# Kernel optimization log

Hardware: AMD Instinct MI355X
Metric: run time of the kernel (lower is better)

The kernel has to match this reference:

```python
import jax, jax.numpy as jnp
import numpy as np

B, S, D, H, OUT = 512, 200, 64, 512, 1
EPS = 1e-5  # torch LayerNorm default


def ln(x, g, b, axes=-1):
    m = x.mean(axis=axes, keepdims=True)
    v = ((x - m) ** 2).mean(axis=axes, keepdims=True)
    return (x - m) * jax.lax.rsqrt(v + EPS) * g + b


def lstm_layer(xs, W_ih, b_ih, W_hh, b_hh, g_ih, be_ih, g_hh, be_hh, g_ho, be_ho):
    # xs: (S, B, in_dim) -> (S, B, H)
    nb = xs.shape[1]
    def step(carry, x_t):
        h, c = carry
        gates = ln(x_t @ W_ih.T + b_ih, g_ih, be_ih) + ln(h @ W_hh.T + b_hh, g_hh, be_hh)
        i, f, g, o = jnp.split(gates, 4, axis=-1)
        c_new = jax.nn.sigmoid(f) * c + jax.nn.sigmoid(i) * jnp.tanh(g)
        h_new = jax.nn.sigmoid(o) * ln(jnp.tanh(c_new), g_ho, be_ho)
        return (h_new, c_new), h_new
    init = (jnp.zeros((nb, H), xs.dtype), jnp.zeros((nb, H), xs.dtype))
    _, hs = jax.lax.scan(step, init, xs)
    return hs


def setup_inputs() -> dict:
    key = jax.random.key(0)
    ks = iter(jax.random.split(key, 16))
    scale = 0.02
    def rn(shape):
        return jax.random.normal(next(ks), shape, jnp.float32) * scale
    inp = {"x": jax.random.normal(next(ks), (B, S, D), jnp.float32)}
    inp["ln1_g"] = jnp.ones((S, D), jnp.float32)
    inp["ln1_b"] = jnp.zeros((S, D), jnp.float32)
    for l, ind in ((0, D), (1, H)):
        inp[f"W_ih{l}"] = rn((4 * H, ind)); inp[f"b_ih{l}"] = jnp.zeros((4 * H,), jnp.float32)
        inp[f"W_hh{l}"] = rn((4 * H, H));  inp[f"b_hh{l}"] = jnp.zeros((4 * H,), jnp.float32)
        inp[f"g_ih{l}"] = jnp.ones((4 * H,), jnp.float32); inp[f"be_ih{l}"] = jnp.zeros((4 * H,), jnp.float32)
        inp[f"g_hh{l}"] = jnp.ones((4 * H,), jnp.float32); inp[f"be_hh{l}"] = jnp.zeros((4 * H,), jnp.float32)
        inp[f"g_ho{l}"] = jnp.ones((H,), jnp.float32);     inp[f"be_ho{l}"] = jnp.zeros((H,), jnp.float32)
    inp["Wd1"] = rn((H // 4, H));      inp["bd1"] = jnp.zeros((H // 4,), jnp.float32)
    inp["Wd2"] = rn((H // 8, H // 4)); inp["bd2"] = jnp.zeros((H // 8,), jnp.float32)
    inp["Wd3"] = rn((H // 16, H // 8)); inp["bd3"] = jnp.zeros((H // 16,), jnp.float32)
    inp["Wd4"] = rn((OUT, H // 16));   inp["bd4"] = jnp.zeros((OUT,), jnp.float32)
    return inp


def _forward(x, ln1_g, ln1_b,
             W_ih0, b_ih0, W_hh0, b_hh0, g_ih0, be_ih0, g_hh0, be_hh0, g_ho0, be_ho0,
             W_ih1, b_ih1, W_hh1, b_hh1, g_ih1, be_ih1, g_hh1, be_hh1, g_ho1, be_ho1,
             Wd1, bd1, Wd2, bd2, Wd3, bd3, Wd4, bd4):
    # ln1 normalizes jointly over (seq_len, input_dim)
    x = ln(x, ln1_g, ln1_b, axes=(-2, -1))
    xs = jnp.transpose(x, (1, 0, 2))  # (S, B, D)
    hs = lstm_layer(xs, W_ih0, b_ih0, W_hh0, b_hh0, g_ih0, be_ih0, g_hh0, be_hh0, g_ho0, be_ho0)
    hs = lstm_layer(hs, W_ih1, b_ih1, W_hh1, b_hh1, g_ih1, be_ih1, g_hh1, be_hh1, g_ho1, be_ho1)
    h_last = hs[-1]  # (B, H): last_num=1, eval-mode dropout is identity
    z = jax.nn.relu(h_last @ Wd1.T + bd1)
    z = jax.nn.relu(z @ Wd2.T + bd2)
    z = jax.nn.relu(z @ Wd3.T + bd3)
    return z @ Wd4.T + bd4  # (B, OUT)


def reference(x, ln1_g, ln1_b,
              W_ih0, b_ih0, W_hh0, b_hh0, g_ih0, be_ih0, g_hh0, be_hh0, g_ho0, be_ho0,
              W_ih1, b_ih1, W_hh1, b_hh1, g_ih1, be_ih1, g_hh1, be_hh1, g_ho1, be_ho1,
              Wd1, bd1, Wd2, bd2, Wd3, bd3, Wd4, bd4):
    return _forward(x, ln1_g, ln1_b,
                    W_ih0, b_ih0, W_hh0, b_hh0, g_ih0, be_ih0, g_hh0, be_hh0, g_ho0, be_ho0,
                    W_ih1, b_ih1, W_hh1, b_hh1, g_ih1, be_ih1, g_hh1, be_hh1, g_ho1, be_ho1,
                    Wd1, bd1, Wd2, bd2, Wd3, bd3, Wd4, bd4)
```

## Files before the change

### kernel.cpp

```cpp
#include <hip/hip_runtime.h>
#include <math.h>

#define BATCH 512
#define SEQ   200
#define DIN   64
#define HID   512
#define GW    2048
#define EPS   1e-5f
#define NREG  4

typedef _Float16 half_t;
typedef half_t half8 __attribute__((ext_vector_type(8)));
typedef float  f32x4  __attribute__((ext_vector_type(4)));
typedef float  f32x16 __attribute__((ext_vector_type(16)));

#define WN0 (2048*64)
#define WN1 (2048*512)
#define WTOT (WN0 + 3*WN1)

__device__ __forceinline__ float sigf(float x){ return 1.0f/(1.0f+expf(-x)); }

__device__ __forceinline__ void block_reduce4(float&a,float&b,float&c,float&d,float* red){
  #pragma unroll
  for(int o=32;o;o>>=1){
    a+=__shfl_down(a,o); b+=__shfl_down(b,o);
    c+=__shfl_down(c,o); d+=__shfl_down(d,o);
  }
  const int lane = threadIdx.x & 63, wid = threadIdx.x>>6;
  if(lane==0){ red[wid*4+0]=a; red[wid*4+1]=b; red[wid*4+2]=c; red[wid*4+3]=d; }
  __syncthreads();
  a = red[0]+red[4]+red[8]+red[12];
  b = red[1]+red[5]+red[9]+red[13];
  c = red[2]+red[6]+red[10]+red[14];
  d = red[3]+red[7]+red[11]+red[15];
  __syncthreads();
}

__global__ __launch_bounds__(256) void ln1_stats(const float* __restrict__ x,
                                                 float* __restrict__ mu,
                                                 float* __restrict__ rs){
  const int b = blockIdx.x;
  const float* xb = x + (size_t)b*SEQ*DIN;
  float s=0, ss=0, d=0, e=0;
  for (int i=threadIdx.x; i<SEQ*DIN; i+=256){ float v=xb[i]; s+=v; ss+=v*v; }
  __shared__ float red[16];
  block_reduce4(s,ss,d,e,red);
  if (threadIdx.x==0){
    float m = s*(1.0f/(SEQ*DIN));
    mu[b] = m;
    rs[b] = rsqrtf(ss*(1.0f/(SEQ*DIN)) - m*m + EPS);
  }
}

__global__ __launch_bounds__(256) void wsplit(
    const float* __restrict__ W0, const float* __restrict__ W1,
    const float* __restrict__ W2, const float* __restrict__ W3,
    half_t* __restrict__ Wh, half_t* __restrict__ Wl)
{
  int i = blockIdx.x*256 + threadIdx.x;
  if (i >= WTOT) return;
  const float* src; int off, Kd;
  if (i < WN0){ src=W0; off=i; Kd=DIN; }
  else {
    int r = (i-WN0)/WN1; off = (i-WN0) - r*WN1; Kd=HID;
    src = (r==0)?W1:((r==1)?W2:W3);
  }
  const int C = Kd>>5;
  int j  = off & 7;
  int l  = (off>>3) & 63;
  int ks = (off>>9) & 1;
  int nf = (off>>10) & 1;
  int pc = off>>11;
  int c  = pc & (C-1);
  int p  = pc >> (Kd==DIN ? 1 : 4);
  int n  = p*64 + nf*32 + (l&31);
  int k  = c*32 + ks*16 + (l>>5)*8 + j;
  float v = src[(size_t)n*Kd + k];
  half_t h = (half_t)v;
  Wh[i] = h;
  Wl[i] = (half_t)(v - (float)h);
}

__global__ __launch_bounds__(256) void tick_mm32(
    const float* __restrict__ x, const float* __restrict__ g1, const float* __restrict__ b1,
    const float* __restrict__ mu, const float* __restrict__ rsg,
    const half_t* __restrict__ h0fh, const half_t* __restrict__ h0fl,
    const half_t* __restrict__ h1fh, const half_t* __restrict__ h1fl,
    const half_t* __restrict__ Wh, const half_t* __restrict__ Wl,
    float* __restrict__ G, int t)
{
  const int z    = blockIdx.z;
  const int tid  = threadIdx.x;
  const int lane = tid & 63;
  const int w    = tid >> 6;
  const int ln31 = lane & 31;
  const int lk8  = (lane >> 5) << 3;

  const int wm0 = blockIdx.y*64 + (w>>1)*32;
  const int wn0 = blockIdx.x*128 + (w&1)*64;
  const int p   = blockIdx.x*2 + (w&1);
  const int mch = wm0 >> 5;

  const half_t* Bh = Wh + WN0; const half_t* Bl = Wl + WN0;
  const half_t* FAh = h0fh;    const half_t* FAl = h0fl;
  int Kd = HID;
  if (z==0){ Bh=Wh; Bl=Wl; Kd=DIN; }
  else if (z==2){ Bh=Wh+WN0+WN1; Bl=Wl+WN0+WN1; }
  else if (z==3){ FAh=h1fh; FAl=h1fl; Bh=Wh+WN0+2*WN1; Bl=Wl+WN0+2*WN1; }

  const int C32 = Kd >> 5;
  const int C16 = Kd >> 4;

  const half_t* Bph = Bh + (size_t)p*C32*2048 + lane*8;
  const half_t* Bpl = Bl + (size_t)p*C32*2048 + lane*8;
  const half_t* Aph = FAh + (size_t)mch*HID*32 + lane*8;
  const half_t* Apl = FAl + (size_t)mch*HID*32 + lane*8;

  const int tq = (t < SEQ) ? t : (SEQ-1);

  const int arow = wm0 + ln31;
  float m_=0.f, r_=0.f;
  const float *xr=nullptr, *gr=nullptr, *br=nullptr;
  if (z==0){
    m_ = mu[arow]; r_ = rsg[arow];
    xr = x  + (size_t)arow*(SEQ*DIN) + (size_t)tq*DIN + lk8;
    gr = g1 + (size_t)tq*DIN + lk8;
    br = b1 + (size_t)tq*DIN + lk8;
  }

  f32x16 acc0 = {0.f,0.f,0.f,0.f,0.f,0.f,0.f,0.f,0.f,0.f,0.f,0.f,0.f,0.f,0.f,0.f};
  f32x16 acc1 = acc0;

  struct Frag { half8 ah, al, bh0, bh1, bl0, bl1; };
  auto loadF = [&](int c16)->Frag{
    Frag f;
    if (z==0){
      const float* xp = xr + c16*16;
      const float* gp = gr + c16*16;
      const float* bp = br + c16*16;
      #pragma unroll
      for (int j=0;j<8;j++){
        float v = (xp[j]-m_)*r_*gp[j] + bp[j];
        half_t hv = (half_t)v;
        f.ah[j] = hv; f.al[j] = (half_t)(v - (float)hv);
      }
    } else {
      f.ah = *(const half8*)(Aph + (size_t)c16*512);
      f.al = *(const half8*)(Apl + (size_t)c16*512);
    }
    const size_t boff = (size_t)(c16>>1)*2048 + (size_t)(c16&1)*512;
    f.bh0 = *(const half8*)(Bph + boff);
    f.bh1 = *(const half8*)(Bph + boff + 1024);
    f.bl0 = *(const half8*)(Bpl + boff);
    f.bl1 = *(const half8*)(Bpl + boff + 1024);
    return f;
  };
  auto mmstep = [&](const Frag& f){
    acc0 = __builtin_amdgcn_mfma_f32_32x32x16_f16(f.ah, f.bh0, acc0, 0,0,0);
    acc1 = __builtin_amdgcn_mfma_f32_32x32x16_f16(f.ah, f.bh1, acc1, 0,0,0);
    acc0 = __builtin_amdgcn_mfma_f32_32x32x16_f16(f.al, f.bh0, acc0, 0,0,0);
    acc1 = __builtin_amdgcn_mfma_f32_32x32x16_f16(f.al, f.bh1, acc1, 0,0,0);
    acc0 = __builtin_amdgcn_mfma_f32_32x32x16_f16(f.ah, f.bl0, acc0, 0,0,0);
    acc1 = __builtin_amdgcn_mfma_f32_32x32x16_f16(f.ah, f.bl1, acc1, 0,0,0);
  };

  Frag Fa = loadF(0);
  for (int c=0; c<C16; c+=2){
    Frag Fb = loadF(c+1);
    mmstep(Fa);
    if (c+2 < C16) Fa = loadF(c+2);
    mmstep(Fb);
  }

  float* Gr = G + (size_t)z*BATCH*GW + (size_t)0;
  const int rbase = (lane>>5)<<2;
  #pragma unroll
  for (int reg=0; reg<16; reg++){
    const int m = wm0 + (reg&3) + ((reg>>2)<<3) + rbase;
    __builtin_nontemporal_store(acc0[reg], &Gr[(size_t)m*GW + wn0 + ln31]);
    __builtin_nontemporal_store(acc1[reg], &Gr[(size_t)m*GW + wn0 + 32 + ln31]);
  }
}

__global__ __launch_bounds__(256) void tick_update(
    const float* __restrict__ G,
    const float* __restrict__ b_ih0, const float* __restrict__ b_hh0,
    const float* __restrict__ b_ih1, const float* __restrict__ b_hh1,
    const float* __restrict__ g_ih0, const float* __restrict__ be_ih0,
    const float* __restrict__ g_hh0, const float* __restrict__ be_hh0,
    const float* __restrict__ g_ho0, const float* __restrict__ be_ho0,
    const float* __restrict__ g_ih1, const float* __restrict__ be_ih1,
    const float* __restrict__ g_hh1, const float* __restrict__ be_hh1,
    const float* __restrict__ g_ho1, const float* __restrict__ be_ho1,
    float* __restrict__ h0, float* __restrict__ c0,
    float* __restrict__ h1, float* __restrict__ c1,
    half_t* __restrict__ h0fh, half_t* __restrict__ h0fl,
    half_t* __restrict__ h1fh, half_t* __restrict__ h1fl, int t)
{
  const int layer = blockIdx.x >> 9;
  const int b = blockIdx.x & 511;
  if (layer==0 && t>=SEQ) return;
  if (layer==1 && t==0)   return;

  const float *GA,*GB,*bA,*bB,*gA,*beA,*gB,*beB,*gH,*bH;
  float *cs,*hs; half_t *hfx,*lfx;
  const size_t rb = (size_t)b*GW;
  if (layer==0){
    GA = G + rb;
    GB = G + (size_t)1*BATCH*GW + rb;
    bA=b_ih0; bB=b_hh0;
    gA=g_ih0; beA=be_ih0; gB=g_hh0; beB=be_hh0; gH=g_ho0; bH=be_ho0;
    cs = c0 + b*HID; hs = h0 + b*HID; hfx = h0fh; lfx = h0fl;
  } else {
    GA = G + (size_t)2*BATCH*GW + rb;
    GB = G + (size_t)3*BATCH*GW + rb;
    bA=b_ih1; bB=b_hh1;
    gA=g_ih1; beA=be_ih1; gB=g_hh1; beB=be_hh1; gH=g_ho1; bH=be_ho1;
    cs = c1 + b*HID; hs = h1 + b*HID; hfx = h1fh; lfx = h1fl;
  }

  const int tid = threadIdx.x;
  __shared__ float red[16];
  __shared__ __align__(16) float GS[2*GW];
  __shared__ float su[HID];
  __shared__ float so[HID];

  float sa=0, ssa=0, sb=0, ssb=0;
  for (int i=tid*4; i<GW; i+=1024){
    f32x4 va = *(const f32x4*)(GA+i);
    va += *(const f32x4*)(bA+i);
    *(f32x4*)(GS+i) = va;
    f32x4 vb = *(const f32x4*)(GB+i);
    vb += *(const f32x4*)(bB+i);
    *(f32x4*)(GS+GW+i) = vb;
    #pragma unroll
    for (int q=0;q<4;q++){
      sa += va[q]; ssa += va[q]*va[q];
      sb += vb[q]; ssb += vb[q]*vb[q];
    }
  }
  block_reduce4(sa,ssa,sb,ssb,red);
  const float ma = sa*(1.0f/GW);
  const float ra = rsqrtf(ssa*(1.0f/GW) - ma*ma + EPS);
  const float mb = sb*(1.0f/GW);
  const float rb_ = rsqrtf(ssb*(1.0f/GW) - mb*mb + EPS);

  float s_u=0, s_uu=0;
  for (int j=tid;j<HID;j+=256){
    float iv = ((GS[j      ]-ma)*ra*gA[j      ]+beA[j      ]) + ((GS[GW+j      ]-mb)*rb_*gB[j      ]+beB[j      ]);
    float fv = ((GS[j+  HID]-ma)*ra*gA[j+  HID]+beA[j+  HID]) + ((GS[GW+j+  HID]-mb)*rb_*gB[j+  HID]+beB[j+  HID]);
    float gv = ((GS[j+2*HID]-ma)*ra*gA[j+2*HID]+beA[j+2*HID]) + ((GS[GW+j+2*HID]-mb)*rb_*gB[j+2*HID]+beB[j+2*HID]);
    float ov = ((GS[j+3*HID]-ma)*ra*gA[j+3*HID]+beA[j+3*HID]) + ((GS[GW+j+3*HID]-mb)*rb_*gB[j+3*HID]+beB[j+3*HID]);
    float cn = sigf(fv)*cs[j] + sigf(iv)*tanhf(gv);
    cs[j] = cn;
    float u = tanhf(cn);
    su[j] = u; so[j] = sigf(ov);
    s_u += u; s_uu += u*u;
  }
  float d3=0,d4=0;
  block_reduce4(s_u,s_uu,d3,d4,red);
  const float mu_u = s_u*(1.0f/HID);
  const float ru   = rsqrtf(s_uu*(1.0f/HID) - mu_u*mu_u + EPS);

  const size_t fbase = ((size_t)(b>>5)*32)*512 + (size_t)(b&31)*8;
  for (int j=tid;j<HID;j+=256){
    float v = so[j] * ((su[j]-mu_u)*ru*gH[j] + bH[j]);
    hs[j] = v;
    half_t hv = (half_t)v;
    half_t lv = (half_t)(v - (float)hv);
    const size_t fi = fbase + (size_t)(j>>4)*512 + (size_t)((j>>3)&1)*256 + (j&7);
    hfx[fi] = hv;
    lfx[fi] = lv;
  }
}

__global__ __launch_bounds__(256) void head_kernel(
    const float* __restrict__ h1,
    const float* __restrict__ Wd1, const float* __restrict__ bd1,
    const float* __restrict__ Wd2, const float* __restrict__ bd2,
    const float* __restrict__ Wd3, const float* __restrict__ bd3,
    const float* __restrict__ Wd4, const float* __restrict__ bd4,
    float* __restrict__ out)
{
  const int b = blockIdx.x;
  __shared__ float hv[HID];
  __shared__ float z1[128];
  __shared__ float z2[64];
  __shared__ float z3[32];
  const int tid = threadIdx.x;
  for (int i=tid;i<HID;i+=256) hv[i]=h1[(size_t)b*HID+i];
  __syncthreads();
  if (tid<128){
    float acc=bd1[tid]; const float* w=Wd1+(size_t)tid*512;
    for(int k=0;k<512;k++) acc+=hv[k]*w[k];
    z1[tid]=fmaxf(acc,0.f);
  }
  __syncthreads();
  if (tid<64){
    float acc=bd2[tid]; const float* w=Wd2+(size_t)tid*128;
    for(int k=0;k<128;k++) acc+=z1[k]*w[k];
    z2[tid]=fmaxf(acc,0.f);
  }
  __syncthreads();
  if (tid<32){
    float acc=bd3[tid]; const float* w=Wd3+(size_t)tid*64;
    for(int k=0;k<64;k++) acc+=z2[k]*w[k];
    z3[tid]=fmaxf(acc,0.f);
  }
  __syncthreads();
  if (tid==0){
    float acc=bd4[0];
    for(int k=0;k<32;k++) acc+=z3[k]*Wd4[k];
    out[b]=acc;
  }
}

extern "C" void kernel_launch(void* const* d_in, const int* in_sizes, int n_in,
                              void* d_out, int out_size, void* d_ws, size_t ws_size,
                              hipStream_t stream) {
  const float* x      = (const float*)d_in[0];
  const float* ln1_g  = (const float*)d_in[1];
  const float* ln1_b  = (const float*)d_in[2];
  const float* W_ih0  = (const float*)d_in[3];
  const float* b_ih0  = (const float*)d_in[4];
  const float* W_hh0  = (const float*)d_in[5];
  const float* b_hh0  = (const float*)d_in[6];
  const float* g_ih0  = (const float*)d_in[7];
  const float* be_ih0 = (const float*)d_in[8];
  const float* g_hh0  = (const float*)d_in[9];
  const float* be_hh0 = (const float*)d_in[10];
  const float* g_ho0  = (const float*)d_in[11];
  const float* be_ho0 = (const float*)d_in[12];
  const float* W_ih1  = (const float*)d_in[13];
  const float* b_ih1  = (const float*)d_in[14];
  const float* W_hh1  = (const float*)d_in[15];
  const float* b_hh1  = (const float*)d_in[16];
  const float* g_ih1  = (const float*)d_in[17];
  const float* be_ih1 = (const float*)d_in[18];
  const float* g_hh1  = (const float*)d_in[19];
  const float* be_hh1 = (const float*)d_in[20];
  const float* g_ho1  = (const float*)d_in[21];
  const float* be_ho1 = (const float*)d_in[22];
  const float* Wd1    = (const float*)d_in[23];
  const float* bd1    = (const float*)d_in[24];
  const float* Wd2    = (const float*)d_in[25];
  const float* bd2    = (const float*)d_in[26];
  const float* Wd3    = (const float*)d_in[27];
  const float* bd3    = (const float*)d_in[28];
  const float* Wd4    = (const float*)d_in[29];
  const float* bd4    = (const float*)d_in[30];
  float* out = (float*)d_out;

  float* ws = (float*)d_ws;
  float* G  = ws;
  float* h0 = G  + NREG*(size_t)BATCH*GW;
  float* c0 = h0 + (size_t)BATCH*HID;
  float* h1 = c0 + (size_t)BATCH*HID;
  float* c1 = h1 + (size_t)BATCH*HID;
  half_t* h0fh = (half_t*)(c1 + (size_t)BATCH*HID);
  half_t* h0fl = h0fh + (size_t)BATCH*HID;
  half_t* h1fh = h0fl + (size_t)BATCH*HID;
  half_t* h1fl = h1fh + (size_t)BATCH*HID;
  float* mu = (float*)(h1fl + (size_t)BATCH*HID);
  float* rs = mu + BATCH;
  half_t* Wh = (half_t*)(rs + BATCH);
  half_t* Wl = Wh + (size_t)WTOT;

  hipMemsetAsync(h0, 0, 4*(size_t)BATCH*HID*4 + 4*(size_t)BATCH*HID*2, stream);

  ln1_stats<<<BATCH, 256, 0, stream>>>(x, mu, rs);
  wsplit<<<(WTOT+255)/256, 256, 0, stream>>>(W_ih0, W_hh0, W_ih1, W_hh1, Wh, Wl);

  dim3 mgrid(16, 8, NREG);
  for (int t = 0; t <= SEQ; ++t) {
    tick_mm32<<<mgrid, 256, 0, stream>>>(x, ln1_g, ln1_b, mu, rs,
        h0fh, h0fl, h1fh, h1fl, Wh, Wl, G, t);
    tick_update<<<dim3(1024), 256, 0, stream>>>(G,
        b_ih0, b_hh0, b_ih1, b_hh1,
        g_ih0, be_ih0, g_hh0, be_hh0, g_ho0, be_ho0,
        g_ih1, be_ih1, g_hh1, be_hh1, g_ho1, be_ho1,
        h0, c0, h1, c1, h0fh, h0fl, h1fh, h1fl, t);
  }
  head_kernel<<<BATCH, 256, 0, stream>>>(h1, Wd1, bd1, Wd2, bd2, Wd3, bd3, Wd4, bd4, out);
}
```

Measured before the change: 6.028 ms.

## Precompute normalized input fragments and enlarge per-wave MFMA tile to 64x64

Adds an xprep kernel that applies the joint layer norm to the input once for all timesteps, splits it into fp16 hi/lo parts, and stores them in MFMA fragment layout. The per-timestep GEMM kernel then only loads these fragments instead of recomputing the normalization every tick. Each wave now computes a 64x64 output tile (two row chunks times two column halves), so every loaded weight fragment is reused across twice as many rows, and the grid is halved. The cost is a larger workspace, more accumulator registers per wave (launch_bounds 256,1), and fewer blocks per launch (256 instead of 512), which lowers parallelism on a many-CU device.

```diff
diff --git a/kernel.cpp b/kernel.cpp
--- a/kernel.cpp
+++ b/kernel.cpp
@@ -17,6 +17,7 @@
 #define WN0 (2048*64)
 #define WN1 (2048*512)
 #define WTOT (WN0 + 3*WN1)
+#define XFRAG ((size_t)SEQ*16*4*512)
 
 __device__ __forceinline__ float sigf(float x){ return 1.0f/(1.0f+expf(-x)); }
 
@@ -81,9 +82,29 @@
   Wl[i] = (half_t)(v - (float)h);
 }
 
-__global__ __launch_bounds__(256) void tick_mm32(
+__global__ __launch_bounds__(256) void xprep(
     const float* __restrict__ x, const float* __restrict__ g1, const float* __restrict__ b1,
-    const float* __restrict__ mu, const float* __restrict__ rsg,
+    const float* __restrict__ mu, const float* __restrict__ rs,
+    half_t* __restrict__ xh, half_t* __restrict__ xl)
+{
+  size_t i = (size_t)blockIdx.x*256 + threadIdx.x;
+  if (i >= XFRAG) return;
+  int j   = (int)(i & 7);
+  int l   = (int)((i>>3) & 63);
+  int c   = (int)((i>>9) & 3);
+  int mch = (int)((i>>11) & 15);
+  int t   = (int)(i>>15);
+  int b   = mch*32 + (l&31);
+  int k   = c*16 + ((l>>5)<<3) + j;
+  float v = (x[(size_t)b*(SEQ*DIN) + t*DIN + k] - mu[b]) * rs[b]
+            * g1[t*DIN+k] + b1[t*DIN+k];
+  half_t h = (half_t)v;
+  xh[i] = h;
+  xl[i] = (half_t)(v - (float)h);
+}
+
+__global__ __launch_bounds__(256, 1) void tick_mm64(
+    const half_t* __restrict__ xh, const half_t* __restrict__ xl,
     const half_t* __restrict__ h0fh, const half_t* __restrict__ h0fl,
     const half_t* __restrict__ h1fh, const half_t* __restrict__ h1fl,
     const half_t* __restrict__ Wh, const half_t* __restrict__ Wl,
@@ -94,91 +115,91 @@
   const int lane = tid & 63;
   const int w    = tid >> 6;
   const int ln31 = lane & 31;
-  const int lk8  = (lane >> 5) << 3;
-
-  const int wm0 = blockIdx.y*64 + (w>>1)*32;
-  const int wn0 = blockIdx.x*128 + (w&1)*64;
-  const int p   = blockIdx.x*2 + (w&1);
-  const int mch = wm0 >> 5;
+
+  const int mch0 = blockIdx.y*2;
+  const int p    = blockIdx.x*4 + w;
+  const int wn0  = p*64;
 
   const half_t* Bh = Wh + WN0; const half_t* Bl = Wl + WN0;
-  const half_t* FAh = h0fh;    const half_t* FAl = h0fl;
   int Kd = HID;
   if (z==0){ Bh=Wh; Bl=Wl; Kd=DIN; }
   else if (z==2){ Bh=Wh+WN0+WN1; Bl=Wl+WN0+WN1; }
-  else if (z==3){ FAh=h1fh; FAl=h1fl; Bh=Wh+WN0+2*WN1; Bl=Wl+WN0+2*WN1; }
+  else if (z==3){ Bh=Wh+WN0+2*WN1; Bl=Wl+WN0+2*WN1; }
 
   const int C32 = Kd >> 5;
   const int C16 = Kd >> 4;
 
   const half_t* Bph = Bh + (size_t)p*C32*2048 + lane*8;
   const half_t* Bpl = Bl + (size_t)p*C32*2048 + lane*8;
-  const half_t* Aph = FAh + (size_t)mch*HID*32 + lane*8;
-  const half_t* Apl = FAl + (size_t)mch*HID*32 + lane*8;
 
   const int tq = (t < SEQ) ? t : (SEQ-1);
-
-  const int arow = wm0 + ln31;
-  float m_=0.f, r_=0.f;
-  const float *xr=nullptr, *gr=nullptr, *br=nullptr;
+  const half_t *Aph0,*Apl0,*Aph1,*Apl1;
   if (z==0){
-    m_ = mu[arow]; r_ = rsg[arow];
-    xr = x  + (size_t)arow*(SEQ*DIN) + (size_t)tq*DIN + lk8;
-    gr = g1 + (size_t)tq*DIN + lk8;
-    br = b1 + (size_t)tq*DIN + lk8;
-  }
-
-  f32x16 acc0 = {0.f,0.f,0.f,0.f,0.f,0.f,0.f,0.f,0.f,0.f,0.f,0.f,0.f,0.f,0.f,0.f};
-  f32x16 acc1 = acc0;
-
-  struct Frag { half8 ah, al, bh0, bh1, bl0, bl1; };
-  auto loadF = [&](int c16)->Frag{
-    Frag f;
-    if (z==0){
-      const float* xp = xr + c16*16;
-      const float* gp = gr + c16*16;
-      const float* bp = br + c16*16;
-      #pragma unroll
-      for (int j=0;j<8;j++){
-        float v = (xp[j]-m_)*r_*gp[j] + bp[j];
-        half_t hv = (half_t)v;
-        f.ah[j] = hv; f.al[j] = (half_t)(v - (float)hv);
-      }
-    } else {
-      f.ah = *(const half8*)(Aph + (size_t)c16*512);
-      f.al = *(const half8*)(Apl + (size_t)c16*512);
-    }
-    const size_t boff = (size_t)(c16>>1)*2048 + (size_t)(c16&1)*512;
-    f.bh0 = *(const half8*)(Bph + boff);
-    f.bh1 = *(const half8*)(Bph + boff + 1024);
-    f.bl0 = *(const half8*)(Bpl + boff);
-    f.bl1 = *(const half8*)(Bpl + boff + 1024);
+    const size_t xb = ((size_t)tq*16 + mch0)*2048 + lane*8;
+    Aph0 = xh + xb; Aph1 = xh + xb + 2048;
+    Apl0 = xl + xb; Apl1 = xl + xb + 2048;
+  } else {
+    const half_t* FAh = (z==3) ? h1fh : h0fh;
+    const half_t* FAl = (z==3) ? h1fl : h0fl;
+    const size_t ab = (size_t)mch0*16384 + lane*8;
+    Aph0 = FAh + ab; Aph1 = FAh + ab + 16384;
+    Apl0 = FAl + ab; Apl1 = FAl + ab + 16384;
+  }
+
+  f32x16 acc00 = {0.f,0.f,0.f,0.f,0.f,0.f,0.f,0.f,0.f,0.f,0.f,0.f,0.f,0.f,0.f,0.f};
+  f32x16 acc01 = acc00, acc10 = acc00, acc11 = acc00;
+
+  struct F { half8 ah0,al0,ah1,al1,bh0,bh1,bl0,bl1; };
+  auto loadF = [&](int c)->F{
+    F f;
+    const size_t ao = (size_t)c*512;
+    f.ah0 = *(const half8*)(Aph0 + ao);
+    f.al0 = *(const half8*)(Apl0 + ao);
+    f.ah1 = *(const half8*)(Aph1 + ao);
+    f.al1 = *(const half8*)(Apl1 + ao);
+    const size_t bo = (size_t)(c>>1)*2048 + (size_t)(c&1)*512;
+    f.bh0 = *(const half8*)(Bph + bo);
+    f.bh1 = *(const half8*)(Bph + bo + 1024);
+    f.bl0 = *(const half8*)(Bpl + bo);
+    f.bl1 = *(const half8*)(Bpl + bo + 1024);
     return f;
   };
-  auto mmstep = [&](const Frag& f){
-    acc0 = __builtin_amdgcn_mfma_f32_32x32x16_f16(f.ah, f.bh0, acc0, 0,0,0);
-    acc1 = __builtin_amdgcn_mfma_f32_32x32x16_f16(f.ah, f.bh1, acc1, 0,0,0);
-    acc0 = __builtin_amdgcn_mfma_f32_32x32x16_f16(f.al, f.bh0, acc0, 0,0,0);
-    acc1 = __builtin_amdgcn_mfma_f32_32x32x16_f16(f.al, f.bh1, acc1, 0,0,0);
-    acc0 = __builtin_amdgcn_mfma_f32_32x32x16_f16(f.ah, f.bl0, acc0, 0,0,0);
-    acc1 = __builtin_amdgcn_mfma_f32_32x32x16_f16(f.ah, f.bl1, acc1, 0,0,0);
+  auto mmstep = [&](const F& f){
+    acc00 = __builtin_amdgcn_mfma_f32_32x32x16_f16(f.ah0, f.bh0, acc00, 0,0,0);
+    acc01 = __builtin_amdgcn_mfma_f32_32x32x16_f16(f.ah0, f.bh1, acc01, 0,0,0);
+    acc10 = __builtin_amdgcn_mfma_f32_32x32x16_f16(f.ah1, f.bh0, acc10, 0,0,0);
+    acc11 = __builtin_amdgcn_mfma_f32_32x32x16_f16(f.ah1, f.bh1, acc11, 0,0,0);
+    acc00 = __builtin_amdgcn_mfma_f32_32x32x16_f16(f.al0, f.bh0, acc00, 0,0,0);
+    acc01 = __builtin_amdgcn_mfma_f32_32x32x16_f16(f.al0, f.bh1, acc01, 0,0,0);
+    acc10 = __builtin_amdgcn_mfma_f32_32x32x16_f16(f.al1, f.bh0, acc10, 0,0,0);
+    acc11 = __builtin_amdgcn_mfma_f32_32x32x16_f16(f.al1, f.bh1, acc11, 0,0,0);
+    acc00 = __builtin_amdgcn_mfma_f32_32x32x16_f16(f.ah0, f.bl0, acc00, 0,0,0);
+    acc01 = __builtin_amdgcn_mfma_f32_32x32x16_f16(f.ah0, f.bl1, acc01, 0,0,0);
+    acc10 = __builtin_amdgcn_mfma_f32_32x32x16_f16(f.ah1, f.bl0, acc10, 0,0,0);
+    acc11 = __builtin_amdgcn_mfma_f32_32x32x16_f16(f.ah1, f.bl1, acc11, 0,0,0);
   };
 
-  Frag Fa = loadF(0);
+  F f0 = loadF(0);
+  F f1 = loadF(1);
   for (int c=0; c<C16; c+=2){
-    Frag Fb = loadF(c+1);
-    mmstep(Fa);
-    if (c+2 < C16) Fa = loadF(c+2);
-    mmstep(Fb);
-  }
-
-  float* Gr = G + (size_t)z*BATCH*GW + (size_t)0;
+    F f2, f3;
+    if (c+2 < C16){ f2 = loadF(c+2); f3 = loadF(c+3); }
+    mmstep(f0);
+    mmstep(f1);
+    f0 = f2; f1 = f3;
+  }
+
+  float* Gr = G + (size_t)z*BATCH*GW;
   const int rbase = (lane>>5)<<2;
   #pragma unroll
   for (int reg=0; reg<16; reg++){
-    const int m = wm0 + (reg&3) + ((reg>>2)<<3) + rbase;
-    __builtin_nontemporal_store(acc0[reg], &Gr[(size_t)m*GW + wn0 + ln31]);
-    __builtin_nontemporal_store(acc1[reg], &Gr[(size_t)m*GW + wn0 + 32 + ln31]);
+    const int row = (reg&3) + ((reg>>2)<<3) + rbase;
+    const int m0 = mch0*32 + row;
+    const int m1 = m0 + 32;
+    __builtin_nontemporal_store(acc00[reg], &Gr[(size_t)m0*GW + wn0 + ln31]);
+    __builtin_nontemporal_store(acc01[reg], &Gr[(size_t)m0*GW + wn0 + 32 + ln31]);
+    __builtin_nontemporal_store(acc10[reg], &Gr[(size_t)m1*GW + wn0 + ln31]);
+    __builtin_nontemporal_store(acc11[reg], &Gr[(size_t)m1*GW + wn0 + 32 + ln31]);
   }
 }
 
@@ -365,15 +386,18 @@
   float* rs = mu + BATCH;
   half_t* Wh = (half_t*)(rs + BATCH);
   half_t* Wl = Wh + (size_t)WTOT;
+  half_t* xh = Wl + (size_t)WTOT;
+  half_t* xl = xh + XFRAG;
 
   hipMemsetAsync(h0, 0, 4*(size_t)BATCH*HID*4 + 4*(size_t)BATCH*HID*2, stream);
 
   ln1_stats<<<BATCH, 256, 0, stream>>>(x, mu, rs);
   wsplit<<<(WTOT+255)/256, 256, 0, stream>>>(W_ih0, W_hh0, W_ih1, W_hh1, Wh, Wl);
-
-  dim3 mgrid(16, 8, NREG);
+  xprep<<<(int)((XFRAG+255)/256), 256, 0, stream>>>(x, ln1_g, ln1_b, mu, rs, xh, xl);
+
+  dim3 mgrid(8, 8, NREG);
   for (int t = 0; t <= SEQ; ++t) {
-    tick_mm32<<<mgrid, 256, 0, stream>>>(x, ln1_g, ln1_b, mu, rs,
+    tick_mm64<<<mgrid, 256, 0, stream>>>(xh, xl,
         h0fh, h0fl, h1fh, h1fl, Wh, Wl, G, t);
     tick_update<<<dim3(1024), 256, 0, stream>>>(G,
         b_ih0, b_hh0, b_ih1, b_hh1,
```

Result: faster. 5.677 ms (-5.8%).
